# Optimization experiments

Hardware: AMD Instinct MI355X
Metric: run time of the kernel (lower is better)

The kernel has to match this reference:

```python
import jax, jax.numpy as jnp
import numpy as np

H = 12          # num_attention_heads
D = 768         # hidden_size
HD = D // H     # attention_head_size = 64
B, S = 2, 4096
NEG = -1e9

def setup_inputs() -> dict:
    key = jax.random.key(0)
    ks = jax.random.split(key, 6)
    scale = 0.02
    inp = {
        'x': jax.random.normal(ks[0], (B, S, D), jnp.float32),
        'mask': jax.random.randint(ks[1], (B, 1, 1, S), 0, 2, jnp.int32),
        'Wq': jax.random.normal(ks[2], (D, D), jnp.float32) * scale,
        'bq': jnp.zeros((D,), jnp.float32),
        'Wk': jax.random.normal(ks[3], (D, D), jnp.float32) * scale,
        'bk': jnp.zeros((D,), jnp.float32),
        'Wv': jax.random.normal(ks[4], (D, D), jnp.float32) * scale,
        'bv': jnp.zeros((D,), jnp.float32),
        'Wo': jax.random.normal(ks[5], (D, D), jnp.float32) * scale,
        'bo': jnp.zeros((D,), jnp.float32),
    }
    return inp

def reference(x, mask, Wq, bq, Wk, bk, Wv, bv, Wo, bo):
    b, s, _ = x.shape
    # QKV projections (torch Linear: y = x @ W^T + b)
    q = (x @ Wq.T + bq).reshape(b, s, H, HD).transpose(0, 2, 1, 3)  # [B,H,S,HD]
    k = (x @ Wk.T + bk).reshape(b, s, H, HD).transpose(0, 2, 1, 3)
    v = (x @ Wv.T + bv).reshape(b, s, H, HD).transpose(0, 2, 1, 3)
    scores = jnp.einsum('bhqd,bhkd->bhqk', q, k) / jnp.sqrt(jnp.float32(HD))
    scores = jnp.where(mask == 0, jnp.float32(NEG), scores)
    attn = jax.nn.softmax(scores, axis=-1)  # dropout is identity in eval
    ctx = jnp.einsum('bhqk,bhkd->bhqd', attn, v)
    ctx = ctx.transpose(0, 2, 1, 3).reshape(b, s, D)
    return ctx @ Wo.T + bo
```

## Files before the change

kernel.cpp:

```cpp
#include <hip/hip_runtime.h>


#define S_LEN 4096
#define NHEAD 12
#define NEGB2 (-1.442695e9f)
#define THR2 11.541561f
#define QSCALE 0.18033688f

typedef __attribute__((ext_vector_type(8))) short short8;
typedef __attribute__((ext_vector_type(4))) float f32x4;
typedef __attribute__((ext_vector_type(4))) int i32x4;

__device__ __forceinline__ unsigned short f2bf(float f) {
  unsigned u = __builtin_bit_cast(unsigned, f);
  u += 0x7fffu + ((u >> 16) & 1u);
  return (unsigned short)(u >> 16);
}

__device__ __forceinline__ f32x4 mfma_bf16(short8 a, short8 b, f32x4 c) {
  return __builtin_amdgcn_mfma_f32_16x16x32_bf16(a, b, c, 0, 0, 0);
}

__global__ __launch_bounds__(64) void mask_scan(const int* __restrict__ mask,
                                                int* __restrict__ pos,
                                                int* __restrict__ cnt) {
  const int b = blockIdx.x;
  const int lane = threadIdx.x;
  const int* mb = mask + b * S_LEN;
  int* pb = pos + b * S_LEN;
  const int base = lane * 64;
  int cntl = 0;
  for (int j = 0; j < 64; j++) cntl += (mb[base + j] != 0);
  int x = cntl;
#pragma unroll
  for (int off = 1; off < 64; off <<= 1) {
    int y = __shfl_up(x, off);
    if (lane >= off) x += y;
  }
  const int total = __shfl(x, 63);
  int o = x - cntl;
  for (int j = 0; j < 64; j++) {
    const int mv = mb[base + j];
    pb[base + j] = (mv != 0) ? o : -1;
    o += (mv != 0);
  }
  if (lane == 0) cnt[b] = total;
}

__global__ __launch_bounds__(256) void cvt_kernel(const float* __restrict__ in,
                                                  unsigned short* __restrict__ out,
                                                  int n8) {
  int i = blockIdx.x * blockDim.x + threadIdx.x;
  int stride = gridDim.x * blockDim.x;
  for (; i < n8; i += stride) {
    float4 a = ((const float4*)in)[i * 2];
    float4 b = ((const float4*)in)[i * 2 + 1];
    short8 r;
    r[0] = (short)f2bf(a.x); r[1] = (short)f2bf(a.y);
    r[2] = (short)f2bf(a.z); r[3] = (short)f2bf(a.w);
    r[4] = (short)f2bf(b.x); r[5] = (short)f2bf(b.y);
    r[6] = (short)f2bf(b.z); r[7] = (short)f2bf(b.w);
    ((short8*)out)[i] = r;
  }
}

__global__ __launch_bounds__(256) void cvt_w4_kernel(const float* __restrict__ w0,
                                                     const float* __restrict__ w1,
                                                     const float* __restrict__ w2,
                                                     const float* __restrict__ w3,
                                                     unsigned short* __restrict__ out,
                                                     int n8) {
  const int k = blockIdx.y;
  const float* in = (k == 0) ? w0 : (k == 1) ? w1 : (k == 2) ? w2 : w3;
  unsigned short* dst = out + (size_t)k * n8 * 8;
  int i = blockIdx.x * blockDim.x + threadIdx.x;
  int stride = gridDim.x * blockDim.x;
  for (; i < n8; i += stride) {
    float4 a = ((const float4*)in)[i * 2];
    float4 b = ((const float4*)in)[i * 2 + 1];
    short8 r;
    r[0] = (short)f2bf(a.x); r[1] = (short)f2bf(a.y);
    r[2] = (short)f2bf(a.z); r[3] = (short)f2bf(a.w);
    r[4] = (short)f2bf(b.x); r[5] = (short)f2bf(b.y);
    r[6] = (short)f2bf(b.z); r[7] = (short)f2bf(b.w);
    ((short8*)dst)[i] = r;
  }
}

template <int EPI>
__global__ __launch_bounds__(256)
void gemm_bt(const unsigned short* __restrict__ A, const unsigned short* __restrict__ Bm,
             int K,
             const float* __restrict__ bias0, const float* __restrict__ bias1,
             const float* __restrict__ bias2, const int* __restrict__ pos,
             unsigned short* __restrict__ qkv_out, float* __restrict__ f_out) {
  __shared__ short As[128][40];
  __shared__ short Bs[128][40];
  const int n0 = blockIdx.x * 128;
  const int m0 = blockIdx.y * 128;
  const int t = threadIdx.x;
  const int lane = t & 63;
  const int w = t >> 6, wm = w >> 1, wn = w & 1;
  const int sr = t >> 2, sc = (t & 3) * 8;
  const unsigned short* ga = A + (m0 + sr) * K + sc;
  const unsigned short* gb = Bm + (n0 + sr) * K + sc;
  f32x4 acc[4][4] = {};
  for (int kt = 0; kt < K; kt += 32) {
    short8 a0 = *(const short8*)(ga + kt);
    short8 a1 = *(const short8*)(ga + kt + 64 * K);
    short8 b0 = *(const short8*)(gb + kt);
    short8 b1 = *(const short8*)(gb + kt + 64 * K);
    __syncthreads();
    *(short8*)&As[sr][sc] = a0;
    *(short8*)&As[sr + 64][sc] = a1;
    *(short8*)&Bs[sr][sc] = b0;
    *(short8*)&Bs[sr + 64][sc] = b1;
    __syncthreads();
    short8 af[4], bfr[4];
#pragma unroll
    for (int i = 0; i < 4; i++) {
      af[i]  = *(const short8*)&As[wm * 64 + i * 16 + (lane & 15)][(lane >> 4) * 8];
      bfr[i] = *(const short8*)&Bs[wn * 64 + i * 16 + (lane & 15)][(lane >> 4) * 8];
    }
#pragma unroll
    for (int mi = 0; mi < 4; mi++)
#pragma unroll
      for (int ni = 0; ni < 4; ni++)
        acc[mi][ni] = mfma_bf16(af[mi], bfr[ni], acc[mi][ni]);
  }
  if constexpr (EPI == 0) {
    const int tix = n0 / 768;
    const float* bias = (tix == 0) ? bias0 : (tix == 1) ? bias1 : bias2;
    unsigned short* dst = qkv_out + tix * (2 * NHEAD * S_LEN * 64);
    if (tix == 0) {
#pragma unroll
      for (int mi = 0; mi < 4; mi++) {
        const int r0 = m0 + wm * 64 + mi * 16 + ((lane >> 4) << 2);
#pragma unroll
        for (int ni = 0; ni < 4; ni++) {
          const int jr = n0 + wn * 64 + ni * 16 + (lane & 15);
          const int h = jr >> 6, d = jr & 63;
          const float bv = bias[jr];
#pragma unroll
          for (int reg = 0; reg < 4; reg++) {
            const int r = r0 + reg;
            const int b = r >> 12, s = r & (S_LEN - 1);
            dst[(((b * NHEAD + h) * S_LEN + s) << 6) + d] =
                f2bf((acc[mi][ni][reg] + bv) * QSCALE);
          }
        }
      }
    } else {
#pragma unroll
      for (int mi = 0; mi < 4; mi++) {
        const int r0 = m0 + wm * 64 + mi * 16 + ((lane >> 4) << 2);
#pragma unroll
        for (int reg = 0; reg < 4; reg++) {
          const int r = r0 + reg;
          const int b = r >> 12, s = r & (S_LEN - 1);
          const int cpos = pos[b * S_LEN + s];
          if (cpos >= 0) {
#pragma unroll
            for (int ni = 0; ni < 4; ni++) {
              const int jr = (n0 - tix * 768) + wn * 64 + ni * 16 + (lane & 15);
              const int h = jr >> 6, d = jr & 63;
              dst[(((b * NHEAD + h) * S_LEN + cpos) << 6) + d] =
                  f2bf(acc[mi][ni][reg] + bias[jr]);
            }
          }
        }
      }
    }
  } else {
#pragma unroll
    for (int mi = 0; mi < 4; mi++) {
      const int r0 = m0 + wm * 64 + mi * 16 + ((lane >> 4) << 2);
#pragma unroll
      for (int ni = 0; ni < 4; ni++) {
        const int gc = n0 + wn * 64 + ni * 16 + (lane & 15);
        const float bv = bias0[gc];
#pragma unroll
        for (int reg = 0; reg < 4; reg++)
          f_out[(r0 + reg) * 768 + gc] = acc[mi][ni][reg] + bv;
      }
    }
  }
}

__global__ __launch_bounds__(256)
void attn_kernel(const unsigned short* __restrict__ Q, const unsigned short* __restrict__ Km,
                 const unsigned short* __restrict__ V, const int* __restrict__ cnt,
                 unsigned short* __restrict__ ctx) {
  __shared__ short Ks[2][64][64];
  __shared__ short Vt[2][64][72];
  __shared__ short Ps[4][32][72];
  const int qt = blockIdx.x;
  const int bh = blockIdx.y;
  const int b = bh / NHEAD, h = bh % NHEAD;
  const unsigned short* Qb = Q + bh * (S_LEN * 64);
  const unsigned short* Kb = Km + bh * (S_LEN * 64);
  const unsigned short* Vb = V + bh * (S_LEN * 64);
  const int t = threadIdx.x, lane = t & 63, w = t >> 6;
  const int c = lane & 15, g = lane >> 4;
  const int q0 = qt * 128 + w * 32;
  const int cntb = cnt[b];
  const int ntiles = (cntb + 63) >> 6;

  short8 qf[2][2];
#pragma unroll
  for (int qi = 0; qi < 2; qi++)
#pragma unroll
    for (int kk = 0; kk < 2; kk++)
      qf[qi][kk] = *(const short8*)(Qb + (q0 + qi * 16 + c) * 64 + kk * 32 + g * 8);

  f32x4 oacc[4][2] = {};
  float mrun[2], lrun[2];
  mrun[0] = mrun[1] = -__builtin_inff();
  lrun[0] = lrun[1] = 0.f;

  const int sr = t >> 3, k8 = t & 7, sc = k8 * 8;
  const int swzw = k8 << 3;
  const int kx = (k8 ^ (sr & 7)) * 8;

  {
    short8 kv0 = *(const short8*)(Kb + sr * 64 + sc);
    short8 kv1 = *(const short8*)(Kb + (sr + 32) * 64 + sc);
    short8 vv0 = *(const short8*)(Vb + sr * 64 + sc);
    short8 vv1 = *(const short8*)(Vb + (sr + 32) * 64 + sc);
    *(short8*)&Ks[0][sr][kx] = kv0;
    *(short8*)&Ks[0][sr + 32][kx] = kv1;
#pragma unroll
    for (int j = 0; j < 8; j++) {
      Vt[0][sc + j][sr ^ swzw] = vv0[j];
      Vt[0][sc + j][(sr + 32) ^ swzw] = vv1[j];
    }
  }
  __syncthreads();

  for (int it = 0; it < ntiles; ++it) {
    const int bd = it & 1;
    const int k0 = it * 64;
    short8 nk0, nk1, nv0, nv1;
    if (it < ntiles - 1) {
      const int kn = k0 + 64;
      nk0 = *(const short8*)(Kb + (kn + sr) * 64 + sc);
      nk1 = *(const short8*)(Kb + (kn + sr + 32) * 64 + sc);
      nv0 = *(const short8*)(Vb + (kn + sr) * 64 + sc);
      nv1 = *(const short8*)(Vb + (kn + sr + 32) * 64 + sc);
    }

    f32x4 st[2][4];
    __builtin_amdgcn_s_setprio(1);
#pragma unroll
    for (int mi = 0; mi < 4; mi++) {
      short8 ka0 = *(const short8*)&Ks[bd][mi * 16 + c][(g ^ (c & 7)) * 8];
      short8 ka1 = *(const short8*)&Ks[bd][mi * 16 + c][((4 + g) ^ (c & 7)) * 8];
#pragma unroll
      for (int qi = 0; qi < 2; qi++) {
        f32x4 zz = {0.f, 0.f, 0.f, 0.f};
        zz = mfma_bf16(ka0, qf[qi][0], zz);
        zz = mfma_bf16(ka1, qf[qi][1], zz);
        st[qi][mi] = zz;
      }
    }
    __builtin_amdgcn_s_setprio(0);
    if (k0 + 64 > cntb) {
#pragma unroll
      for (int mi = 0; mi < 4; mi++)
#pragma unroll
        for (int r = 0; r < 4; r++) {
          const float pb = (k0 + 16 * mi + 4 * g + r >= cntb) ? NEGB2 : 0.f;
          st[0][mi][r] += pb;
          st[1][mi][r] += pb;
        }
    }
    float pm[2];
#pragma unroll
    for (int qi = 0; qi < 2; qi++) {
      float x = st[qi][0][0];
#pragma unroll
      for (int mi = 0; mi < 4; mi++)
#pragma unroll
        for (int r = 0; r < 4; r++) x = fmaxf(x, st[qi][mi][r]);
      x = fmaxf(x, __shfl_xor(x, 16));
      x = fmaxf(x, __shfl_xor(x, 32));
      pm[qi] = x;
    }
    if (!__all((pm[0] <= mrun[0] + THR2) && (pm[1] <= mrun[1] + THR2))) {
#pragma unroll
      for (int qi = 0; qi < 2; qi++) {
        float mnew = fmaxf(mrun[qi], pm[qi]);
        float al = __builtin_amdgcn_exp2f(mrun[qi] - mnew);
        mrun[qi] = mnew;
        lrun[qi] *= al;
#pragma unroll
        for (int dmi = 0; dmi < 4; dmi++)
#pragma unroll
          for (int r = 0; r < 4; r++) oacc[dmi][qi][r] *= al;
      }
    }
#pragma unroll
    for (int qi = 0; qi < 2; qi++) {
      float ps = 0.f;
#pragma unroll
      for (int mi = 0; mi < 4; mi++)
#pragma unroll
        for (int r = 0; r < 4; r++) {
          float p = __builtin_amdgcn_exp2f(st[qi][mi][r] - mrun[qi]);
          st[qi][mi][r] = p;
          ps += p;
        }
      ps += __shfl_xor(ps, 16);
      ps += __shfl_xor(ps, 32);
      lrun[qi] += ps;
    }
#pragma unroll
    for (int qi = 0; qi < 2; qi++)
#pragma unroll
      for (int mi = 0; mi < 4; mi++) {
        unsigned u0, u1;
        asm("v_cvt_pk_bf16_f32 %0, %1, %2"
            : "=v"(u0) : "v"(st[qi][mi][0]), "v"(st[qi][mi][1]));
        asm("v_cvt_pk_bf16_f32 %0, %1, %2"
            : "=v"(u1) : "v"(st[qi][mi][2]), "v"(st[qi][mi][3]));
        uint2 uv; uv.x = u0; uv.y = u1;
        *(uint2*)&Ps[w][16 * qi + c][16 * mi + 4 * g] = uv;
      }
#pragma unroll
    for (int kk = 0; kk < 2; kk++) {
      short8 pb[2];
#pragma unroll
      for (int qi = 0; qi < 2; qi++)
        pb[qi] = *(const short8*)&Ps[w][16 * qi + c][32 * kk + 8 * g];
      __builtin_amdgcn_s_setprio(1);
#pragma unroll
      for (int dmi = 0; dmi < 4; dmi++) {
        const int hsw = ((2 * dmi + (c >> 3)) & 7) << 3;
        short8 vf = *(const short8*)&Vt[bd][16 * dmi + c][(32 * kk + 8 * g) ^ hsw];
        oacc[dmi][0] = mfma_bf16(vf, pb[0], oacc[dmi][0]);
        oacc[dmi][1] = mfma_bf16(vf, pb[1], oacc[dmi][1]);
      }
      __builtin_amdgcn_s_setprio(0);
    }
    if (it < ntiles - 1) {
      *(short8*)&Ks[bd ^ 1][sr][kx] = nk0;
      *(short8*)&Ks[bd ^ 1][sr + 32][kx] = nk1;
#pragma unroll
      for (int j = 0; j < 8; j++) {
        Vt[bd ^ 1][sc + j][sr ^ swzw] = nv0[j];
        Vt[bd ^ 1][sc + j][(sr + 32) ^ swzw] = nv1[j];
      }
    }
    __syncthreads();
  }
#pragma unroll
  for (int qi = 0; qi < 2; qi++) {
    const float inv = 1.f / lrun[qi];
    const int row = q0 + qi * 16 + c;
#pragma unroll
    for (int dmi = 0; dmi < 4; dmi++) {
      float x0 = oacc[dmi][qi][0] * inv, x1 = oacc[dmi][qi][1] * inv;
      float x2 = oacc[dmi][qi][2] * inv, x3 = oacc[dmi][qi][3] * inv;
      unsigned p0, p1;
      asm("v_cvt_pk_bf16_f32 %0, %1, %2" : "=v"(p0) : "v"(x0), "v"(x1));
      asm("v_cvt_pk_bf16_f32 %0, %1, %2" : "=v"(p1) : "v"(x2), "v"(x3));
      uint2 u2v; u2v.x = p0; u2v.y = p1;
      *(uint2*)&ctx[(size_t)(b * S_LEN + row) * 768 + h * 64 + 16 * dmi + 4 * g] = u2v;
    }
  }
}

extern "C" void kernel_launch(void* const* d_in, const int* in_sizes, int n_in,
                              void* d_out, int out_size, void* d_ws, size_t ws_size,
                              hipStream_t stream) {
  const float* x  = (const float*)d_in[0];
  const int* mask = (const int*)d_in[1];
  const float* Wq = (const float*)d_in[2];
  const float* bq = (const float*)d_in[3];
  const float* Wk = (const float*)d_in[4];
  const float* bk = (const float*)d_in[5];
  const float* Wv = (const float*)d_in[6];
  const float* bv = (const float*)d_in[7];
  const float* Wo = (const float*)d_in[8];
  const float* bo = (const float*)d_in[9];
  float* out = (float*)d_out;

  const int NE = 8192 * 768;
  const int WE = 768 * 768;
  unsigned short* ws   = (unsigned short*)d_ws;
  unsigned short* xb   = ws;
  unsigned short* wqkv = xb + NE;
  unsigned short* wob  = wqkv + 3 * WE;
  unsigned short* qb   = wob + WE;
  unsigned short* ctxb = qb + 3 * NE;
  int* pos = (int*)(ctxb + NE);
  int* cnt = pos + 2 * S_LEN;

  mask_scan<<<dim3(2), 64, 0, stream>>>(mask, pos, cnt);
  cvt_kernel<<<dim3(2048), 256, 0, stream>>>(x, xb, NE / 8);
  cvt_w4_kernel<<<dim3(288, 4), 256, 0, stream>>>(Wq, Wk, Wv, Wo, wqkv, WE / 8);

  gemm_bt<0><<<dim3(18, 64), 256, 0, stream>>>(xb, wqkv, 768, bq, bk, bv, pos,
                                               qb, nullptr);
  attn_kernel<<<dim3(32, 24), 256, 0, stream>>>(qb, qb + NE, qb + 2 * NE, cnt, ctxb);
  gemm_bt<1><<<dim3(6, 64), 256, 0, stream>>>(ctxb, wob, 768, bo, nullptr, nullptr,
                                              nullptr, nullptr, out);
}
```

Before: 300.1 us.

## Use direct global-to-LDS loads, pre-transposed V, and register permlane P-shuffle

Both the projection GEMM and the attention kernel now stage tiles with global_load_lds (direct global-to-LDS DMA), double-buffered with XOR-swizzled layouts, so operands no longer pass through registers and one barrier per iteration is dropped. The V projection epilogue writes V already transposed ([b,h,d,s]), which removes the scalar LDS transpose the attention kernel did on every tile. The P matrix is rearranged into MFMA operand layout with permlane32/16 swaps in registers instead of a round trip through a per-wave LDS buffer. The cost is strided scattered stores when writing transposed V, plus reliance on gfx950 instructions and on correct swizzle and barrier placement.

After: 299.1 us. About the same (-0.3%).

```diff
diff --git a/kernel.cpp b/kernel.cpp
--- a/kernel.cpp
+++ b/kernel.cpp
@@ -19,6 +19,12 @@
 
 __device__ __forceinline__ f32x4 mfma_bf16(short8 a, short8 b, f32x4 c) {
   return __builtin_amdgcn_mfma_f32_16x16x32_bf16(a, b, c, 0, 0, 0);
+}
+
+__device__ __forceinline__ void gload16(const void* g, void* l) {
+  __builtin_amdgcn_global_load_lds(
+      (const __attribute__((address_space(1))) void*)g,
+      (__attribute__((address_space(3))) void*)l, 16, 0, 0);
 }
 
 __global__ __launch_bounds__(64) void mask_scan(const int* __restrict__ mask,
@@ -94,33 +100,42 @@
              const float* __restrict__ bias0, const float* __restrict__ bias1,
              const float* __restrict__ bias2, const int* __restrict__ pos,
              unsigned short* __restrict__ qkv_out, float* __restrict__ f_out) {
-  __shared__ short As[128][40];
-  __shared__ short Bs[128][40];
+  __shared__ short As[2][128][32];
+  __shared__ short Bs[2][128][32];
   const int n0 = blockIdx.x * 128;
   const int m0 = blockIdx.y * 128;
   const int t = threadIdx.x;
   const int lane = t & 63;
   const int w = t >> 6, wm = w >> 1, wn = w & 1;
-  const int sr = t >> 2, sc = (t & 3) * 8;
-  const unsigned short* ga = A + (m0 + sr) * K + sc;
-  const unsigned short* gb = Bm + (n0 + sr) * K + sc;
+  const int c = lane & 15, g = lane >> 4;
+  const int srow = t >> 2, sch = t & 3;
+
   f32x4 acc[4][4] = {};
-  for (int kt = 0; kt < K; kt += 32) {
-    short8 a0 = *(const short8*)(ga + kt);
-    short8 a1 = *(const short8*)(ga + kt + 64 * K);
-    short8 b0 = *(const short8*)(gb + kt);
-    short8 b1 = *(const short8*)(gb + kt + 64 * K);
+  const int nk = K >> 5;
+
+#define G_STAGE(bsel, kt)                                                     \
+  {                                                                           \
+    _Pragma("unroll") for (int p = 0; p < 2; p++) {                           \
+      const int row = p * 64 + srow;                                          \
+      const int gcol = (kt) + ((sch ^ ((row >> 1) & 3)) * 8);                 \
+      gload16(A + (size_t)(m0 + row) * K + gcol,                              \
+              (char*)&As[bsel][0][0] + p * 4096 + (t >> 6) * 1024);           \
+      gload16(Bm + (size_t)(n0 + row) * K + gcol,                             \
+              (char*)&Bs[bsel][0][0] + p * 4096 + (t >> 6) * 1024);           \
+    }                                                                         \
+  }
+
+  G_STAGE(0, 0);
+  for (int kt = 0; kt < nk; kt++) {
+    const int cur = kt & 1;
     __syncthreads();
-    *(short8*)&As[sr][sc] = a0;
-    *(short8*)&As[sr + 64][sc] = a1;
-    *(short8*)&Bs[sr][sc] = b0;
-    *(short8*)&Bs[sr + 64][sc] = b1;
-    __syncthreads();
+    if (kt + 1 < nk) G_STAGE(cur ^ 1, (kt + 1) << 5);
+    const int sw = (c >> 1) & 3;
     short8 af[4], bfr[4];
 #pragma unroll
     for (int i = 0; i < 4; i++) {
-      af[i]  = *(const short8*)&As[wm * 64 + i * 16 + (lane & 15)][(lane >> 4) * 8];
-      bfr[i] = *(const short8*)&Bs[wn * 64 + i * 16 + (lane & 15)][(lane >> 4) * 8];
+      af[i]  = *(const short8*)&As[cur][wm * 64 + i * 16 + c][(g ^ sw) * 8];
+      bfr[i] = *(const short8*)&Bs[cur][wn * 64 + i * 16 + c][(g ^ sw) * 8];
     }
 #pragma unroll
     for (int mi = 0; mi < 4; mi++)
@@ -128,6 +143,8 @@
       for (int ni = 0; ni < 4; ni++)
         acc[mi][ni] = mfma_bf16(af[mi], bfr[ni], acc[mi][ni]);
   }
+#undef G_STAGE
+
   if constexpr (EPI == 0) {
     const int tix = n0 / 768;
     const float* bias = (tix == 0) ? bias0 : (tix == 1) ? bias1 : bias2;
@@ -135,10 +152,10 @@
     if (tix == 0) {
 #pragma unroll
       for (int mi = 0; mi < 4; mi++) {
-        const int r0 = m0 + wm * 64 + mi * 16 + ((lane >> 4) << 2);
+        const int r0 = m0 + wm * 64 + mi * 16 + (g << 2);
 #pragma unroll
         for (int ni = 0; ni < 4; ni++) {
-          const int jr = n0 + wn * 64 + ni * 16 + (lane & 15);
+          const int jr = n0 + wn * 64 + ni * 16 + c;
           const int h = jr >> 6, d = jr & 63;
           const float bv = bias[jr];
 #pragma unroll
@@ -150,10 +167,10 @@
           }
         }
       }
-    } else {
+    } else if (tix == 1) {
 #pragma unroll
       for (int mi = 0; mi < 4; mi++) {
-        const int r0 = m0 + wm * 64 + mi * 16 + ((lane >> 4) << 2);
+        const int r0 = m0 + wm * 64 + mi * 16 + (g << 2);
 #pragma unroll
         for (int reg = 0; reg < 4; reg++) {
           const int r = r0 + reg;
@@ -162,7 +179,7 @@
           if (cpos >= 0) {
 #pragma unroll
             for (int ni = 0; ni < 4; ni++) {
-              const int jr = (n0 - tix * 768) + wn * 64 + ni * 16 + (lane & 15);
+              const int jr = (n0 - 768) + wn * 64 + ni * 16 + c;
               const int h = jr >> 6, d = jr & 63;
               dst[(((b * NHEAD + h) * S_LEN + cpos) << 6) + d] =
                   f2bf(acc[mi][ni][reg] + bias[jr]);
@@ -170,14 +187,34 @@
           }
         }
       }
+    } else {
+#pragma unroll
+      for (int mi = 0; mi < 4; mi++) {
+        const int r0 = m0 + wm * 64 + mi * 16 + (g << 2);
+#pragma unroll
+        for (int reg = 0; reg < 4; reg++) {
+          const int r = r0 + reg;
+          const int b = r >> 12, s = r & (S_LEN - 1);
+          const int cpos = pos[b * S_LEN + s];
+          if (cpos >= 0) {
+#pragma unroll
+            for (int ni = 0; ni < 4; ni++) {
+              const int jr = (n0 - 1536) + wn * 64 + ni * 16 + c;
+              const int h = jr >> 6, d = jr & 63;
+              dst[((size_t)((b * NHEAD + h) * 64 + d) << 12) + cpos] =
+                  f2bf(acc[mi][ni][reg] + bias[jr]);
+            }
+          }
+        }
+      }
     }
   } else {
 #pragma unroll
     for (int mi = 0; mi < 4; mi++) {
-      const int r0 = m0 + wm * 64 + mi * 16 + ((lane >> 4) << 2);
+      const int r0 = m0 + wm * 64 + mi * 16 + (g << 2);
 #pragma unroll
       for (int ni = 0; ni < 4; ni++) {
-        const int gc = n0 + wn * 64 + ni * 16 + (lane & 15);
+        const int gc = n0 + wn * 64 + ni * 16 + c;
         const float bv = bias0[gc];
 #pragma unroll
         for (int reg = 0; reg < 4; reg++)
@@ -189,22 +226,22 @@
 
 __global__ __launch_bounds__(256)
 void attn_kernel(const unsigned short* __restrict__ Q, const unsigned short* __restrict__ Km,
-                 const unsigned short* __restrict__ V, const int* __restrict__ cnt,
+                 const unsigned short* __restrict__ Vtg, const int* __restrict__ cnt,
                  unsigned short* __restrict__ ctx) {
   __shared__ short Ks[2][64][64];
-  __shared__ short Vt[2][64][72];
-  __shared__ short Ps[4][32][72];
+  __shared__ short Vt[2][64][64];
   const int qt = blockIdx.x;
   const int bh = blockIdx.y;
   const int b = bh / NHEAD, h = bh % NHEAD;
   const unsigned short* Qb = Q + bh * (S_LEN * 64);
   const unsigned short* Kb = Km + bh * (S_LEN * 64);
-  const unsigned short* Vb = V + bh * (S_LEN * 64);
+  const unsigned short* Vb = Vtg + (size_t)bh * 64 * S_LEN;
   const int t = threadIdx.x, lane = t & 63, w = t >> 6;
   const int c = lane & 15, g = lane >> 4;
   const int q0 = qt * 128 + w * 32;
   const int cntb = cnt[b];
   const int ntiles = (cntb + 63) >> 6;
+  const bool lo32 = (lane < 32);
 
   short8 qf[2][2];
 #pragma unroll
@@ -218,36 +255,27 @@
   mrun[0] = mrun[1] = -__builtin_inff();
   lrun[0] = lrun[1] = 0.f;
 
-  const int sr = t >> 3, k8 = t & 7, sc = k8 * 8;
-  const int swzw = k8 << 3;
-  const int kx = (k8 ^ (sr & 7)) * 8;
-
-  {
-    short8 kv0 = *(const short8*)(Kb + sr * 64 + sc);
-    short8 kv1 = *(const short8*)(Kb + (sr + 32) * 64 + sc);
-    short8 vv0 = *(const short8*)(Vb + sr * 64 + sc);
-    short8 vv1 = *(const short8*)(Vb + (sr + 32) * 64 + sc);
-    *(short8*)&Ks[0][sr][kx] = kv0;
-    *(short8*)&Ks[0][sr + 32][kx] = kv1;
-#pragma unroll
-    for (int j = 0; j < 8; j++) {
-      Vt[0][sc + j][sr ^ swzw] = vv0[j];
-      Vt[0][sc + j][(sr + 32) ^ swzw] = vv1[j];
-    }
-  }
-  __syncthreads();
+  const int srow = t >> 3, sch = t & 7;
+
+#define A_STAGE(bsel, k0v)                                                    \
+  {                                                                           \
+    _Pragma("unroll") for (int p = 0; p < 2; p++) {                           \
+      const int row = p * 32 + srow;                                          \
+      const int gc8 = ((sch ^ (row & 7)) * 8);                                \
+      gload16(Kb + (size_t)((k0v) + row) * 64 + gc8,                          \
+              (char*)&Ks[bsel][0][0] + p * 4096 + (t >> 6) * 1024);           \
+      gload16(Vb + (size_t)row * S_LEN + (k0v) + gc8,                         \
+              (char*)&Vt[bsel][0][0] + p * 4096 + (t >> 6) * 1024);           \
+    }                                                                         \
+  }
+
+  A_STAGE(0, 0);
 
   for (int it = 0; it < ntiles; ++it) {
     const int bd = it & 1;
     const int k0 = it * 64;
-    short8 nk0, nk1, nv0, nv1;
-    if (it < ntiles - 1) {
-      const int kn = k0 + 64;
-      nk0 = *(const short8*)(Kb + (kn + sr) * 64 + sc);
-      nk1 = *(const short8*)(Kb + (kn + sr + 32) * 64 + sc);
-      nv0 = *(const short8*)(Vb + (kn + sr) * 64 + sc);
-      nv1 = *(const short8*)(Vb + (kn + sr + 32) * 64 + sc);
-    }
+    __syncthreads();
+    if (it + 1 < ntiles) A_STAGE(bd ^ 1, k0 + 64);
 
     f32x4 st[2][4];
     __builtin_amdgcn_s_setprio(1);
@@ -299,6 +327,7 @@
           for (int r = 0; r < 4; r++) oacc[dmi][qi][r] *= al;
       }
     }
+    unsigned uu[2][4][2];
 #pragma unroll
     for (int qi = 0; qi < 2; qi++) {
       float ps = 0.f;
@@ -313,46 +342,44 @@
       ps += __shfl_xor(ps, 16);
       ps += __shfl_xor(ps, 32);
       lrun[qi] += ps;
-    }
-#pragma unroll
-    for (int qi = 0; qi < 2; qi++)
 #pragma unroll
       for (int mi = 0; mi < 4; mi++) {
-        unsigned u0, u1;
         asm("v_cvt_pk_bf16_f32 %0, %1, %2"
-            : "=v"(u0) : "v"(st[qi][mi][0]), "v"(st[qi][mi][1]));
+            : "=v"(uu[qi][mi][0]) : "v"(st[qi][mi][0]), "v"(st[qi][mi][1]));
         asm("v_cvt_pk_bf16_f32 %0, %1, %2"
-            : "=v"(u1) : "v"(st[qi][mi][2]), "v"(st[qi][mi][3]));
-        uint2 uv; uv.x = u0; uv.y = u1;
-        *(uint2*)&Ps[w][16 * qi + c][16 * mi + 4 * g] = uv;
-      }
+            : "=v"(uu[qi][mi][1]) : "v"(st[qi][mi][2]), "v"(st[qi][mi][3]));
+      }
+    }
 #pragma unroll
     for (int kk = 0; kk < 2; kk++) {
       short8 pb[2];
 #pragma unroll
-      for (int qi = 0; qi < 2; qi++)
-        pb[qi] = *(const short8*)&Ps[w][16 * qi + c][32 * kk + 8 * g];
+      for (int qi = 0; qi < 2; qi++) {
+        i32x4 dw;
+#pragma unroll
+        for (int x = 0; x < 2; x++) {
+          unsigned pa = uu[qi][2 * kk][x], qa = pa;
+          asm("v_permlane32_swap_b32 %0, %1" : "+v"(pa), "+v"(qa));
+          asm("v_permlane16_swap_b32 %0, %1" : "+v"(pa), "+v"(qa));
+          unsigned pbr = uu[qi][2 * kk + 1][x], qbr = pbr;
+          asm("v_permlane32_swap_b32 %0, %1" : "+v"(pbr), "+v"(qbr));
+          asm("v_permlane16_swap_b32 %0, %1" : "+v"(pbr), "+v"(qbr));
+          dw[x]     = (int)(lo32 ? pa : pbr);
+          dw[2 + x] = (int)(lo32 ? qa : qbr);
+        }
+        pb[qi] = __builtin_bit_cast(short8, dw);
+      }
       __builtin_amdgcn_s_setprio(1);
 #pragma unroll
       for (int dmi = 0; dmi < 4; dmi++) {
-        const int hsw = ((2 * dmi + (c >> 3)) & 7) << 3;
-        short8 vf = *(const short8*)&Vt[bd][16 * dmi + c][(32 * kk + 8 * g) ^ hsw];
+        short8 vf = *(const short8*)&Vt[bd][16 * dmi + c][((4 * kk + g) ^ (c & 7)) * 8];
         oacc[dmi][0] = mfma_bf16(vf, pb[0], oacc[dmi][0]);
         oacc[dmi][1] = mfma_bf16(vf, pb[1], oacc[dmi][1]);
       }
       __builtin_amdgcn_s_setprio(0);
     }
-    if (it < ntiles - 1) {
-      *(short8*)&Ks[bd ^ 1][sr][kx] = nk0;
-      *(short8*)&Ks[bd ^ 1][sr + 32][kx] = nk1;
-#pragma unroll
-      for (int j = 0; j < 8; j++) {
-        Vt[bd ^ 1][sc + j][sr ^ swzw] = nv0[j];
-        Vt[bd ^ 1][sc + j][(sr + 32) ^ swzw] = nv1[j];
-      }
-    }
-    __syncthreads();
-  }
+  }
+#undef A_STAGE
 #pragma unroll
   for (int qi = 0; qi < 2; qi++) {
     const float inv = 1.f / lrun[qi];
```
